# Performance work log

Measured on AMD Instinct MI355X. Metric: run time of the kernel, lower is better.

The kernel has to match this reference:

```python
import jax, jax.numpy as jnp
import numpy as np

IC = 8      # inter_channels = in_channels // 2
K = 5       # top-k
EPS = 1e-5  # BatchNorm eps


def _conv(x, w, b, stride, pad):
    y = jax.lax.conv_general_dilated(
        x, w, (stride, stride), [(pad, pad), (pad, pad)],
        dimension_numbers=('NCHW', 'OIHW', 'NCHW'))
    return y + b[None, :, None, None]


def _maxpool2(x):
    return jax.lax.reduce_window(x, -jnp.inf, jax.lax.max,
                                 (1, 1, 2, 2), (1, 1, 2, 2), 'VALID')


def _up2(x):
    return jnp.repeat(jnp.repeat(x, 2, axis=2), 2, axis=3)


def setup_inputs() -> dict:
    key = jax.random.key(0)
    ks = jax.random.split(key, 12)
    C = 16
    x_ms = jax.random.normal(ks[0], (1, C, 96, 96), jnp.float32)
    hp_pan = jax.random.normal(ks[1], (1, C, 192, 192), jnp.float32)
    x_pan = jax.random.normal(ks[2], (1, C, 192, 192), jnp.float32)
    s = 0.05
    return {
        'x_ms': x_ms, 'hp_pan': hp_pan, 'x_pan': x_pan,
        'g_w': jax.random.normal(ks[3], (IC, C, 1, 1), jnp.float32) * s,
        'g_b': jax.random.normal(ks[4], (IC,), jnp.float32) * s,
        'theta_w': jax.random.normal(ks[5], (IC, C, 3, 3), jnp.float32) * s,
        'theta_b': jax.random.normal(ks[6], (IC,), jnp.float32) * s,
        'phi_w': jax.random.normal(ks[7], (IC, C, 3, 3), jnp.float32) * s,
        'phi_b': jax.random.normal(ks[8], (IC,), jnp.float32) * s,
        'W_w': jax.random.normal(ks[9], (C, IC, 1, 1), jnp.float32) * s,
        'W_b': jax.random.normal(ks[10], (C,), jnp.float32) * s,
        'bn_gamma': jax.random.normal(ks[11], (C,), jnp.float32) * s + 1.0,
        'bn_beta': jnp.zeros((C,), jnp.float32),
    }


def reference(x_ms, hp_pan, x_pan, g_w, g_b, theta_w, theta_b,
              phi_w, phi_b, W_w, W_b, bn_gamma, bn_beta):
    B, _, H, W = x_ms.shape
    # g: 1x1 conv + maxpool2 on hp_pan -> (B, M, IC)
    g_x = _maxpool2(_conv(hp_pan, g_w, g_b, 1, 0))
    g_x = g_x.reshape(B, IC, -1).transpose(0, 2, 1)
    # theta: 3x3 s2 conv + up2 on x_ms -> (B, N, IC), N = H*W
    th = _up2(_conv(x_ms, theta_w, theta_b, 2, 1))
    th = th.reshape(B, IC, -1).transpose(0, 2, 1)
    # phi: 3x3 s2 conv + maxpool2 + up2 on x_pan -> (B, IC, M)
    ph = _up2(_maxpool2(_conv(x_pan, phi_w, phi_b, 2, 1)))
    ph = ph.reshape(B, IC, -1)
    # dense similarity (B, N, M)
    f = jnp.einsum('bnc,bcm->bnm', th, ph)
    scores, idx = jax.lax.top_k(f, K)            # (B, N, K)
    scores = jax.nn.softmax(scores, axis=-1)
    # weighted matmul with V restricted to top-k columns (same math as
    # scatter-into-zeros followed by dense matmul, without the dense zeros)
    bi = jnp.arange(B)[:, None, None]
    g_sel = g_x[bi, idx]                          # (B, N, K, IC)
    y = jnp.einsum('bnk,bnkc->bnc', scores, g_sel)
    y = y.transpose(0, 2, 1).reshape(B, IC, H, W)
    wy = _conv(y, W_w, W_b, 1, 0)
    # BatchNorm2d (training-mode batch statistics)
    mean = wy.mean(axis=(0, 2, 3), keepdims=True)
    var = wy.var(axis=(0, 2, 3), keepdims=True)
    z = (wy - mean) * jax.lax.rsqrt(var + EPS)
    z = z * bn_gamma[None, :, None, None] + bn_beta[None, :, None, None]
    return (z, x_pan)
```

## Files before the change

kernel.cpp:

```cpp
#include <hip/hip_runtime.h>

#define IC 8
#define NC 2304
#define NF 9216
#define Z_ELEMS 147456
#define XPAN_ELEMS 589824

typedef unsigned int uint_t;

__global__ __launch_bounds__(256) void k1_prep(
    const float* __restrict__ xms,
    const float* __restrict__ hppan,
    const float* __restrict__ xpan,
    const float* __restrict__ gw, const float* __restrict__ gb,
    const float* __restrict__ thw, const float* __restrict__ thb,
    const float* __restrict__ phw, const float* __restrict__ phb,
    float* __restrict__ theta_c,
    float* __restrict__ phi_c,
    float* __restrict__ gmat,
    float* __restrict__ xpan_out)
{
    const int b = blockIdx.x;
    const int tid = threadIdx.x;

    if (b < 9) {
        int pix = b * 256 + tid;
        int r = pix / 48, c = pix % 48;
        int ir0 = 2 * r - 1, ic0 = 2 * c - 1;
        bool rok = (r > 0), cok = (c > 0);
        float acc[8];
        #pragma unroll
        for (int co = 0; co < 8; ++co) acc[co] = thb[co];
        #pragma unroll 4
        for (int ci = 0; ci < 16; ++ci) {
            const float* base = xms + ci * 9216;
            float xv[9];
            #pragma unroll
            for (int dr = 0; dr < 3; ++dr) {
                #pragma unroll
                for (int dc = 0; dc < 3; ++dc) {
                    bool ok = (dr > 0 || rok) && (dc > 0 || cok);
                    int off = (ir0 + dr) * 96 + (ic0 + dc);
                    float v = base[ok ? off : 0];
                    xv[dr * 3 + dc] = ok ? v : 0.0f;
                }
            }
            #pragma unroll
            for (int tap = 0; tap < 9; ++tap) {
                #pragma unroll
                for (int co = 0; co < 8; ++co)
                    acc[co] += thw[co * 144 + ci * 9 + tap] * xv[tap];
            }
        }
        #pragma unroll
        for (int co = 0; co < 8; ++co) theta_c[pix * 8 + co] = acc[co];
    } else if (b < 45) {
        int idx = (b - 9) * 256 + tid;
        int cp = idx >> 2, sp = idx & 3;
        int rc = cp / 48, cc = cp % 48;
        int r96 = 2 * rc + (sp >> 1), c96 = 2 * cc + (sp & 1);
        int ir0 = 2 * r96 - 1, ic0 = 2 * c96 - 1;
        bool rok = (r96 > 0), cok = (c96 > 0);
        float acc[8];
        #pragma unroll
        for (int co = 0; co < 8; ++co) acc[co] = 0.0f;
        #pragma unroll 4
        for (int ci = 0; ci < 16; ++ci) {
            const float* base = xpan + ci * 36864;
            float xv[9];
            #pragma unroll
            for (int dr = 0; dr < 3; ++dr) {
                #pragma unroll
                for (int dc = 0; dc < 3; ++dc) {
                    bool ok = (dr > 0 || rok) && (dc > 0 || cok);
                    int off = (ir0 + dr) * 192 + (ic0 + dc);
                    float v = base[ok ? off : 0];
                    xv[dr * 3 + dc] = ok ? v : 0.0f;
                }
            }
            #pragma unroll
            for (int tap = 0; tap < 9; ++tap) {
                #pragma unroll
                for (int co = 0; co < 8; ++co)
                    acc[co] += phw[co * 144 + ci * 9 + tap] * xv[tap];
            }
        }
        #pragma unroll
        for (int co = 0; co < 8; ++co) {
            float v = acc[co];
            v = fmaxf(v, __shfl_xor(v, 1));
            v = fmaxf(v, __shfl_xor(v, 2));
            if (sp == 0) phi_c[cp * 8 + co] = v + phb[co];
        }
    } else if (b < 189) {
        int idx = (b - 45) * 256 + tid;
        int op = idx >> 2, sp = idx & 3;
        int r = 2 * (op / 96) + (sp >> 1), c = 2 * (op % 96) + (sp & 1);
        const float* bp = hppan + r * 192 + c;
        float acc[8];
        #pragma unroll
        for (int co = 0; co < 8; ++co) acc[co] = 0.0f;
        #pragma unroll
        for (int ci = 0; ci < 16; ++ci) {
            float xv = bp[ci * 36864];
            #pragma unroll
            for (int co = 0; co < 8; ++co)
                acc[co] += gw[co * 16 + ci] * xv;
        }
        #pragma unroll
        for (int co = 0; co < 8; ++co) {
            float v = acc[co];
            v = fmaxf(v, __shfl_xor(v, 1));
            v = fmaxf(v, __shfl_xor(v, 2));
            if (sp == 0) gmat[op * 8 + co] = v + gb[co];
        }
    } else {
        int i = (b - 189) * 256 + tid;
        ((uint4*)xpan_out)[i] = ((const uint4*)xpan)[i];
    }
}

__global__ __launch_bounds__(256) void k2_attn(
    const float* __restrict__ theta_c, const float* __restrict__ phi_c,
    const float* __restrict__ gmat, float* __restrict__ y_c)
{
    const int tid = threadIdx.x;
    const int wv = tid >> 6, lane = tid & 63;
    const int nc0 = blockIdx.x * 4;

    float th[4][8];
    #pragma unroll
    for (int r = 0; r < 4; ++r)
        #pragma unroll
        for (int j = 0; j < 8; ++j)
            th[r][j] = theta_c[(nc0 + r) * 8 + j];

    float v1[4], v2[4];
    int i1[4], i2[4];
    #pragma unroll
    for (int r = 0; r < 4; ++r) {
        v1[r] = -INFINITY; v2[r] = -INFINITY;
        i1[r] = 0x7fffffff; i2[r] = 0x7fffffff;
    }

    #pragma unroll
    for (int it = 0; it < 9; ++it) {
        int mc = lane + ((it * 4 + wv) << 6);
        const float4* p = (const float4*)(phi_c + mc * 8);
        float4 a = p[0], bq = p[1];
        #pragma unroll
        for (int r = 0; r < 4; ++r) {
            float v = th[r][0] * a.x + th[r][1] * a.y + th[r][2] * a.z + th[r][3] * a.w
                    + th[r][4] * bq.x + th[r][5] * bq.y + th[r][6] * bq.z + th[r][7] * bq.w;
            if (v > v1[r])      { v2[r] = v1[r]; i2[r] = i1[r]; v1[r] = v; i1[r] = mc; }
            else if (v > v2[r]) { v2[r] = v; i2[r] = mc; }
        }
    }

    #pragma unroll
    for (int r = 0; r < 4; ++r) {
        #pragma unroll
        for (int off = 1; off < 64; off <<= 1) {
            float ov1 = __shfl_xor(v1[r], off);
            int   oi1 = __shfl_xor(i1[r], off);
            float ov2 = __shfl_xor(v2[r], off);
            int   oi2 = __shfl_xor(i2[r], off);
            bool afirst = (v1[r] > ov1) || (v1[r] == ov1 && i1[r] < oi1);
            if (afirst) {
                bool t = (v2[r] > ov1) || (v2[r] == ov1 && i2[r] < oi1);
                v2[r] = t ? v2[r] : ov1; i2[r] = t ? i2[r] : oi1;
            } else {
                bool t = (ov2 > v1[r]) || (ov2 == v1[r] && oi2 < i1[r]);
                float nv2 = t ? ov2 : v1[r]; int ni2 = t ? oi2 : i1[r];
                v1[r] = ov1; i1[r] = oi1; v2[r] = nv2; i2[r] = ni2;
            }
        }
    }

    __shared__ float cv1[4][4], cv2[4][4];
    __shared__ int   ci1[4][4], ci2[4][4];
    if (lane == 0) {
        #pragma unroll
        for (int r = 0; r < 4; ++r) {
            cv1[wv][r] = v1[r]; ci1[wv][r] = i1[r];
            cv2[wv][r] = v2[r]; ci2[wv][r] = i2[r];
        }
    }
    __syncthreads();

    if (tid < 32) {
        int r = tid >> 3, ch = tid & 7;
        float m1 = -INFINITY, m2 = -INFINITY;
        int j1 = 0x7fffffff, j2 = 0x7fffffff;
        #pragma unroll
        for (int w = 0; w < 4; ++w) {
            #pragma unroll
            for (int s = 0; s < 2; ++s) {
                float v = s ? cv2[w][r] : cv1[w][r];
                int   i = s ? ci2[w][r] : ci1[w][r];
                bool b1 = (v > m1) || (v == m1 && i < j1);
                bool b2 = (v > m2) || (v == m2 && i < j2);
                if (b1)      { m2 = m1; j2 = j1; m1 = v; j1 = i; }
                else if (b2) { m2 = v; j2 = i; }
            }
        }
        int rc1 = j1 / 48, cc1 = j1 % 48;
        int m00 = (2 * rc1) * 96 + 2 * cc1;
        int rc2 = j2 / 48, cc2 = j2 % 48;
        int mm2 = (2 * rc2) * 96 + 2 * cc2;
        float e = __expf(m2 - m1);
        float inv = 1.0f / (4.0f + e);
        float gs = gmat[m00 * 8 + ch] + gmat[(m00 + 1) * 8 + ch]
                 + gmat[(m00 + 96) * 8 + ch] + gmat[(m00 + 97) * 8 + ch];
        y_c[(nc0 + r) * 8 + ch] = inv * gs + (e * inv) * gmat[mm2 * 8 + ch];
    }
}

__global__ __launch_bounds__(256) void k3_out(
    const float* __restrict__ y_c,
    const float* __restrict__ Ww, const float* __restrict__ Wb,
    const float* __restrict__ gamma, const float* __restrict__ beta,
    float* __restrict__ zout)
{
    const int co = blockIdx.x;
    const int tid = threadIdx.x;
    float w[8];
    #pragma unroll
    for (int j = 0; j < 8; ++j) w[j] = Ww[co * 8 + j];
    const float bias = Wb[co];

    float wy[9];
    float s = 0.f, s2 = 0.f;
    #pragma unroll
    for (int j = 0; j < 9; ++j) {
        int mc = tid + j * 256;
        const float4* p = (const float4*)(y_c + mc * 8);
        float4 a = p[0], bq = p[1];
        float v = bias + w[0] * a.x + w[1] * a.y + w[2] * a.z + w[3] * a.w
                       + w[4] * bq.x + w[5] * bq.y + w[6] * bq.z + w[7] * bq.w;
        wy[j] = v; s += v; s2 += v * v;
    }
    #pragma unroll
    for (int off = 32; off; off >>= 1) {
        s  += __shfl_down(s, off);
        s2 += __shfl_down(s2, off);
    }
    __shared__ float ps[4], ps2[4];
    __shared__ float sc_s, sh_s;
    int wv = tid >> 6, lane = tid & 63;
    if (lane == 0) { ps[wv] = s; ps2[wv] = s2; }
    __syncthreads();
    if (tid == 0) {
        float S  = ps[0] + ps[1] + ps[2] + ps[3];
        float S2 = ps2[0] + ps2[1] + ps2[2] + ps2[3];
        float mean = S * (1.0f / 2304.0f);
        float var  = S2 * (1.0f / 2304.0f) - mean * mean;
        float rsig = 1.0f / sqrtf(var + 1e-5f);
        float gm = gamma[co], be = beta[co];
        sc_s = gm * rsig;
        sh_s = be - mean * gm * rsig;
    }
    __syncthreads();
    float sc = sc_s, sh = sh_s;
    #pragma unroll
    for (int j = 0; j < 9; ++j) {
        int mc = tid + j * 256;
        int rc = mc / 48, cc = mc % 48;
        float zv = wy[j] * sc + sh;
        float2 zz = make_float2(zv, zv);
        int base = co * 9216 + (2 * rc) * 96 + 2 * cc;
        *(float2*)(zout + base) = zz;
        *(float2*)(zout + base + 96) = zz;
    }
}

extern "C" void kernel_launch(void* const* d_in, const int* in_sizes, int n_in,
                              void* d_out, int out_size, void* d_ws, size_t ws_size,
                              hipStream_t stream) {
    const float* xms   = (const float*)d_in[0];
    const float* hppan = (const float*)d_in[1];
    const float* xpan  = (const float*)d_in[2];
    const float* gw    = (const float*)d_in[3];
    const float* gb    = (const float*)d_in[4];
    const float* thw   = (const float*)d_in[5];
    const float* thb   = (const float*)d_in[6];
    const float* phw   = (const float*)d_in[7];
    const float* phb   = (const float*)d_in[8];
    const float* Ww    = (const float*)d_in[9];
    const float* Wb    = (const float*)d_in[10];
    const float* gam   = (const float*)d_in[11];
    const float* bet   = (const float*)d_in[12];

    float* zout     = (float*)d_out;
    float* xpan_out = zout + Z_ELEMS;

    float* theta_c = (float*)d_ws;
    float* phi_c   = theta_c + NC * IC;
    float* gmat    = phi_c + NC * IC;
    float* y_c     = gmat + NF * IC;

    k1_prep<<<765, 256, 0, stream>>>(xms, hppan, xpan, gw, gb, thw, thb,
                                     phw, phb, theta_c, phi_c, gmat, xpan_out);
    k2_attn<<<576, 256, 0, stream>>>(theta_c, phi_c, gmat, y_c);
    k3_out<<<16, 256, 0, stream>>>(y_c, Ww, Wb, gam, bet, zout);
}
```

Measured before the change: 118.8 us.

## Split conv input channels across thread pairs and move x_pan copy to final kernel

The theta and phi 3x3 convolutions now give each output two threads. Each thread accumulates half of the 16 input channels, and the partial sums are combined with a lane shuffle before the maxpool reduction. This doubles the thread count for the heaviest convolution work in the prep kernel and shortens each thread's serial chain. The x_pan passthrough copy moves out of the prep kernel into extra blocks of the final BN kernel, where it can overlap with the small 16-block BN work instead of competing with the convolutions. The cost is more shuffle instructions and some duplicated index arithmetic.

After: 113.9 us (median of 2 runs). 4.1% less time.

```diff
diff --git a/kernel.cpp b/kernel.cpp
--- a/kernel.cpp
+++ b/kernel.cpp
@@ -17,22 +17,24 @@
     const float* __restrict__ phw, const float* __restrict__ phb,
     float* __restrict__ theta_c,
     float* __restrict__ phi_c,
-    float* __restrict__ gmat,
-    float* __restrict__ xpan_out)
+    float* __restrict__ gmat)
 {
     const int b = blockIdx.x;
     const int tid = threadIdx.x;
 
-    if (b < 9) {
-        int pix = b * 256 + tid;
+    if (b < 18) {
+        int idx = b * 256 + tid;
+        int pix = idx >> 1, half = idx & 1;
         int r = pix / 48, c = pix % 48;
         int ir0 = 2 * r - 1, ic0 = 2 * c - 1;
         bool rok = (r > 0), cok = (c > 0);
         float acc[8];
         #pragma unroll
-        for (int co = 0; co < 8; ++co) acc[co] = thb[co];
+        for (int co = 0; co < 8; ++co) acc[co] = 0.0f;
+        int ci0 = half * 8;
         #pragma unroll 4
-        for (int ci = 0; ci < 16; ++ci) {
+        for (int ci8 = 0; ci8 < 8; ++ci8) {
+            int ci = ci0 + ci8;
             const float* base = xms + ci * 9216;
             float xv[9];
             #pragma unroll
@@ -53,10 +55,13 @@
             }
         }
         #pragma unroll
-        for (int co = 0; co < 8; ++co) theta_c[pix * 8 + co] = acc[co];
-    } else if (b < 45) {
-        int idx = (b - 9) * 256 + tid;
-        int cp = idx >> 2, sp = idx & 3;
+        for (int co = 0; co < 8; ++co) {
+            float v = acc[co] + __shfl_xor(acc[co], 1);
+            if (half == 0) theta_c[pix * 8 + co] = v + thb[co];
+        }
+    } else if (b < 90) {
+        int idx = (b - 18) * 256 + tid;
+        int half = idx & 1, sp = (idx >> 1) & 3, cp = idx >> 3;
         int rc = cp / 48, cc = cp % 48;
         int r96 = 2 * rc + (sp >> 1), c96 = 2 * cc + (sp & 1);
         int ir0 = 2 * r96 - 1, ic0 = 2 * c96 - 1;
@@ -64,8 +69,10 @@
         float acc[8];
         #pragma unroll
         for (int co = 0; co < 8; ++co) acc[co] = 0.0f;
+        int ci0 = half * 8;
         #pragma unroll 4
-        for (int ci = 0; ci < 16; ++ci) {
+        for (int ci8 = 0; ci8 < 8; ++ci8) {
+            int ci = ci0 + ci8;
             const float* base = xpan + ci * 36864;
             float xv[9];
             #pragma unroll
@@ -87,13 +94,13 @@
         }
         #pragma unroll
         for (int co = 0; co < 8; ++co) {
-            float v = acc[co];
-            v = fmaxf(v, __shfl_xor(v, 1));
+            float v = acc[co] + __shfl_xor(acc[co], 1);
             v = fmaxf(v, __shfl_xor(v, 2));
-            if (sp == 0) phi_c[cp * 8 + co] = v + phb[co];
-        }
-    } else if (b < 189) {
-        int idx = (b - 45) * 256 + tid;
+            v = fmaxf(v, __shfl_xor(v, 4));
+            if ((idx & 7) == 0) phi_c[cp * 8 + co] = v + phb[co];
+        }
+    } else {
+        int idx = (b - 90) * 256 + tid;
         int op = idx >> 2, sp = idx & 3;
         int r = 2 * (op / 96) + (sp >> 1), c = 2 * (op % 96) + (sp & 1);
         const float* bp = hppan + r * 192 + c;
@@ -114,9 +121,6 @@
             v = fmaxf(v, __shfl_xor(v, 2));
             if (sp == 0) gmat[op * 8 + co] = v + gb[co];
         }
-    } else {
-        int i = (b - 189) * 256 + tid;
-        ((uint4*)xpan_out)[i] = ((const uint4*)xpan)[i];
     }
 }
 
@@ -220,10 +224,19 @@
     const float* __restrict__ y_c,
     const float* __restrict__ Ww, const float* __restrict__ Wb,
     const float* __restrict__ gamma, const float* __restrict__ beta,
-    float* __restrict__ zout)
+    const float* __restrict__ xpan,
+    float* __restrict__ zout, float* __restrict__ xpan_out)
 {
-    const int co = blockIdx.x;
+    const int b = blockIdx.x;
     const int tid = threadIdx.x;
+
+    if (b >= 16) {
+        int i = (b - 16) * 256 + tid;
+        ((uint4*)xpan_out)[i] = ((const uint4*)xpan)[i];
+        return;
+    }
+
+    const int co = b;
     float w[8];
     #pragma unroll
     for (int j = 0; j < 8; ++j) w[j] = Ww[co * 8 + j];
@@ -299,8 +312,9 @@
     float* gmat    = phi_c + NC * IC;
     float* y_c     = gmat + NF * IC;
 
-    k1_prep<<<765, 256, 0, stream>>>(xms, hppan, xpan, gw, gb, thw, thb,
-                                     phw, phb, theta_c, phi_c, gmat, xpan_out);
+    k1_prep<<<234, 256, 0, stream>>>(xms, hppan, xpan, gw, gb, thw, thb,
+                                     phw, phb, theta_c, phi_c, gmat);
     k2_attn<<<576, 256, 0, stream>>>(theta_c, phi_c, gmat, y_c);
-    k3_out<<<16, 256, 0, stream>>>(y_c, Ww, Wb, gam, bet, zout);
+    k3_out<<<592, 256, 0, stream>>>(y_c, Ww, Wb, gam, bet, xpan,
+                                    zout, xpan_out);
 }
```
